# Kernel tuning notes

Hardware: AMD Instinct MI355X
Metric: run time of the kernel (lower is better)

Reference implementation:

```python
import jax, jax.numpy as jnp
import numpy as np
from jax import lax

N, M, T, IN, H, DEPTH = 64, 10, 160, 40, 256, 3
B = N * M
EPS = 1e-8


def setup_inputs() -> dict:
    key = jax.random.key(0)
    ks = jax.random.split(key, 20)
    s = 1.0 / np.sqrt(H)  # torch LSTM init scale
    inp = {
        "sequences": jax.random.normal(ks[0], (B, T, IN), jnp.float32),
        "len_sequences": jax.random.randint(ks[1], (B,), 80, T + 1, jnp.int32),
        "w_sim": jnp.float32(0.5),
        "b_sim": jnp.float32(0.5),
    }
    in_sizes = [IN, H, H]
    for l in range(DEPTH):
        k = 2 + 4 * l
        inp[f"Wih{l}"] = jax.random.uniform(ks[k], (4 * H, in_sizes[l]), jnp.float32, -s, s)
        inp[f"Whh{l}"] = jax.random.uniform(ks[k + 1], (4 * H, H), jnp.float32, -s, s)
        inp[f"bih{l}"] = jax.random.uniform(ks[k + 2], (4 * H,), jnp.float32, -s, s)
        inp[f"bhh{l}"] = jax.random.uniform(ks[k + 3], (4 * H,), jnp.float32, -s, s)
    return inp


def _lstm_layer(x_tbf, mask_tb, Wih, Whh, bih, bhh):
    """x_tbf: [T,B,F] time-major. mask_tb: [T,B] valid-step mask.
    Returns (h_seq [T,B,H], c_last [B,H]) where c_last is the cell state at
    the last valid timestep of each sequence (packed-sequence semantics)."""
    b = x_tbf.shape[1]
    h0 = jnp.zeros((b, H), x_tbf.dtype)
    c0 = jnp.zeros((b, H), x_tbf.dtype)

    def step(carry, xm):
        h, c = carry
        xt, mt = xm
        g = xt @ Wih.T + bih + h @ Whh.T + bhh  # [B,4H]
        i, f, gg, o = jnp.split(g, 4, axis=1)
        cn = jax.nn.sigmoid(f) * c + jax.nn.sigmoid(i) * jnp.tanh(gg)
        hn = jax.nn.sigmoid(o) * jnp.tanh(cn)
        m = mt[:, None]
        h2 = jnp.where(m, hn, h)
        c2 = jnp.where(m, cn, c)
        return (h2, c2), h2

    (hT, cT), h_seq = lax.scan(step, (h0, c0), (x_tbf, mask_tb))
    return h_seq, cT


def reference(sequences, len_sequences, Wih0, Whh0, bih0, bhh0,
              Wih1, Whh1, bih1, bhh1, Wih2, Whh2, bih2, bhh2,
              w_sim, b_sim):
    lens = len_sequences.astype(jnp.int32)
    x = jnp.transpose(sequences, (1, 0, 2))  # [T,B,IN]
    mask = jnp.arange(T)[:, None] < lens[None, :]  # [T,B]

    layers = [(Wih0, Whh0, bih0, bhh0), (Wih1, Whh1, bih1, bhh1), (Wih2, Whh2, bih2, bhh2)]
    c_last = None
    for (Wih, Whh, bih, bhh) in layers:
        x, c_last = _lstm_layer(x, mask, Wih, Whh, bih, bhh)
    E = c_last  # [B,H] final-layer cell state per utterance (original order)

    # L2-normalize embeddings (F.normalize, p=2, dim=1)
    E = E / jnp.maximum(jnp.linalg.norm(E, axis=1, keepdims=True), 1e-12)

    Er = E.reshape(N, M, H)
    C = Er.mean(axis=1)  # [N,H] speaker centroids
    # exclusive centroids exactly as source: (M*c_j + E_i)/(M-1)
    Cm = ((M * C[:, None, :] + Er) / (M - 1)).reshape(B, H)

    En = E / jnp.maximum(jnp.linalg.norm(E, axis=1, keepdims=True), EPS)
    Cn = C / jnp.maximum(jnp.linalg.norm(C, axis=1, keepdims=True), EPS)
    Cmn = Cm / jnp.maximum(jnp.linalg.norm(Cm, axis=1, keepdims=True), EPS)

    S = (En @ Cn.T) * w_sim + b_sim  # [B,N]: cos(E_i, c_j)*w + b

    # diagonal block: row i, col i//M uses exclusive centroid
    d = jnp.sum(En * Cmn, axis=1)  # [B]
    rows = jnp.arange(B)
    cols = jnp.repeat(jnp.arange(N), M)
    S = S.at[rows, cols].set(d * w_sim + b_sim)
    return S


if __name__ == "__main__":
    out = reference(**setup_inputs())
    print(out.shape, out.dtype)
```

## Files before the change

kernel.cpp:

```cpp
#include <hip/hip_runtime.h>
#include <cstdint>
#include <cstddef>

typedef __attribute__((ext_vector_type(8))) short short8;
typedef __attribute__((ext_vector_type(4))) float f32x4;
typedef __attribute__((ext_vector_type(4))) unsigned short us4;

#define N_SPK 64
#define M_UTT 10
#define T_SEQ 160
#define IN_F  40
#define H_DIM 256
#define B_TOT 640
#define G4    1024

__device__ __forceinline__ unsigned short f2bf(float f) {
  unsigned int u = __float_as_uint(f);
  u += 0x7FFFu + ((u >> 16) & 1u);
  return (unsigned short)(u >> 16);
}
__device__ __forceinline__ float b2f(unsigned short u) {
  return __uint_as_float(((unsigned int)u) << 16);
}
__device__ __forceinline__ float sigm(float x) {
  return 1.f / (1.f + __expf(-x));
}
__device__ __forceinline__ float tanh_fast(float x) {
  return 1.f - 2.f / (1.f + __expf(2.f * x));
}
__device__ __forceinline__ unsigned long long ato_ld(const unsigned long long* p) {
  return __hip_atomic_load(p, __ATOMIC_RELAXED, __HIP_MEMORY_SCOPE_AGENT);
}
__device__ __forceinline__ void ato_st(unsigned long long* p, unsigned long long v) {
  __hip_atomic_store(p, v, __ATOMIC_RELAXED, __HIP_MEMORY_SCOPE_AGENT);
}
__device__ __forceinline__ int flg_ld(const int* p) {
  return __hip_atomic_load(p, __ATOMIC_RELAXED, __HIP_MEMORY_SCOPE_AGENT);
}
__device__ __forceinline__ void flg_st(int* p, int v) {
  __hip_atomic_store(p, v, __ATOMIC_RELAXED, __HIP_MEMORY_SCOPE_AGENT);
}

__global__ void pack_w_kernel(const float* __restrict__ W, short* __restrict__ out,
                              int Kin, int Ktiles) {
  int idx = blockIdx.x * 256 + threadIdx.x;
  int total = 64 * Ktiles * 64;
  if (idx >= total) return;
  int lane = idx & 63;
  int rest = idx >> 6;
  int ks   = rest % Ktiles;
  int tile = rest / Ktiles;
  int n  = tile * 16 + (lane & 15);
  int k0 = ks * 32 + (lane >> 4) * 8;
  short8 v;
#pragma unroll
  for (int j = 0; j < 8; ++j) {
    int k = k0 + j;
    float f = (k < Kin) ? W[(size_t)n * Kin + k] : 0.f;
    v[j] = (short)f2bf(f);
  }
  *(short8*)&out[(size_t)idx * 8] = v;
}

__global__ void bias_sum_kernel(const float* __restrict__ a, const float* __restrict__ b,
                                float* __restrict__ o) {
  int i = blockIdx.x * 256 + threadIdx.x;
  if (i < G4) o[i] = a[i] + b[i];
}

__global__ __launch_bounds__(256, 2)
void gate_gemm0(const float* __restrict__ seq, const short* __restrict__ Wp,
                const float* __restrict__ bias, unsigned short* __restrict__ G) {
  const int btile = blockIdx.x % 40;
  const int rest  = blockIdx.x / 40;
  const int tg    = rest & 3;
  const int chunk = rest >> 2;
  const int tid = threadIdx.x, lane = tid & 63, wave = tid >> 6;
  const int nl = lane & 15, mq = lane >> 4;

  for (int mg = 0; mg < 4; ++mg) {
    const int t0 = chunk * 16 + mg * 4;
    f32x4 acc[4][4];
#pragma unroll
    for (int q = 0; q < 4; ++q) {
      int tile = tg * 16 + wave + 4 * q;
      float bv = bias[tile * 16 + nl];
#pragma unroll
      for (int mm = 0; mm < 4; ++mm) acc[mm][q] = (f32x4){bv, bv, bv, bv};
    }
    for (int kt = 0; kt < 2; ++kt) {
      short8 a[4];
      const int m = btile * 16 + nl;
      const int k0 = kt * 32 + mq * 8;
#pragma unroll
      for (int mm = 0; mm < 4; ++mm) {
#pragma unroll
        for (int j = 0; j < 8; ++j) {
          int k = k0 + j;
          float f = (k < IN_F) ? seq[((size_t)m * T_SEQ + (t0 + mm)) * IN_F + k] : 0.f;
          a[mm][j] = (short)f2bf(f);
        }
      }
#pragma unroll
      for (int q = 0; q < 4; ++q) {
        int tile = tg * 16 + wave + 4 * q;
        short8 b = *(const short8*)&Wp[(((size_t)tile * 2 + kt) * 64 + lane) * 8];
#pragma unroll
        for (int mm = 0; mm < 4; ++mm)
          acc[mm][q] = __builtin_amdgcn_mfma_f32_16x16x32_bf16(a[mm], b, acc[mm][q], 0, 0, 0);
      }
    }
#pragma unroll
    for (int mm = 0; mm < 4; ++mm)
#pragma unroll
      for (int q = 0; q < 4; ++q) {
        int tile = tg * 16 + wave + 4 * q;
        us4 o;
#pragma unroll
        for (int r = 0; r < 4; ++r) o[r] = f2bf(acc[mm][q][r]);
        *(us4*)&G[(((size_t)(t0 + mm) * 40 + btile) * 64 + tile) * 256 + lane * 4] = o;
      }
  }
}

template<int L>
__device__ __forceinline__ void rec_stage(
    int S, int hb,
    const short* __restrict__ Whhp, const short* __restrict__ Wihp,
    const unsigned short* __restrict__ G0, const float* __restrict__ biasl,
    unsigned long long* __restrict__ hxch, int* __restrict__ flags,
    const int* __restrict__ lens, float* __restrict__ c_state,
    unsigned short* h_sh, unsigned short* x_sh, float* c_sh,
    float* bias_sh, short* wih_lds, int* len_sh)
{
  const int tid = threadIdx.x, lane = tid & 63, wave = tid >> 6;
  const int mq = lane >> 4, nl = lane & 15;
  const int lc = wave * 16 + nl;
  const int colown = hb * 64 + lc;

  short8 wregH[4][8];
#pragma unroll
  for (int g = 0; g < 4; ++g) {
    const int tile = g * 16 + hb * 4 + wave;
#pragma unroll
    for (int kt = 0; kt < 8; ++kt)
      wregH[g][kt] = *(const short8*)&Whhp[(((size_t)tile * 8 + kt) * 64 + lane) * 8];
  }
  short8 wregI[4][4];
  if (L >= 1) {
#pragma unroll
    for (int g = 0; g < 4; ++g) {
      const int tile = g * 16 + hb * 4 + wave;
#pragma unroll
      for (int kt = 0; kt < 4; ++kt)
        wregI[g][kt] = *(const short8*)&Wihp[(((size_t)tile * 8 + kt) * 64 + lane) * 8];
    }
    for (int i = tid; i < 4096; i += 256) {
      int tl = i >> 6, ln = i & 63;
      int lt = tl >> 2, kt4 = tl & 3;
      int gt = (lt >> 2) * 16 + hb * 4 + (lt & 3);
      *(short8*)&wih_lds[(lt * 4 + kt4) * 512 + ln * 8] =
          *(const short8*)&Wihp[(((size_t)gt * 8 + 4 + kt4) * 64 + ln) * 8];
    }
    for (int i = tid; i < 1024; i += 256) bias_sh[i] = biasl[i];
  }
  for (int i = tid; i < 64 * 264; i += 256) h_sh[i] = 0;
  for (int i = tid; i < 64 * 65; i += 256) c_sh[i] = 0.f;
  if (tid < 64) len_sh[tid] = lens[S * 64 + tid];
  __syncthreads();

  const int fself = L * 40 + S * 4 + hb;

  for (int t = 0; t < T_SEQ; ++t) {
    const int par = t & 3;
    if (L >= 1 && tid < 4)
      while (flg_ld(&flags[(L - 1) * 40 + S * 4 + tid]) < t + 1) {}
    if (L < 2 && tid >= 4 && tid < 8)
      while (flg_ld(&flags[(L + 1) * 40 + S * 4 + (tid - 4)]) < t - 3) {}
    __syncthreads();

    unsigned long long xr[16];
    if (L >= 1) {
      const unsigned long long* xb =
          hxch + ((size_t)((par * 3 + (L - 1)) * 10 + S)) * 4096;
#pragma unroll
      for (int u = 0; u < 16; ++u) xr[u] = ato_ld(&xb[u * 256 + tid]);
    }
    f32x4 acc[4][4];
    if (L == 0) {
#pragma unroll
      for (int m = 0; m < 4; ++m)
#pragma unroll
        for (int g = 0; g < 4; ++g) {
          const int tile = g * 16 + hb * 4 + wave;
          us4 gv = *(const us4*)&G0[(((size_t)t * 40 + S * 4 + m) * 64 + tile) * 256 + lane * 4];
#pragma unroll
          for (int r = 0; r < 4; ++r) acc[m][g][r] = b2f(gv[r]);
        }
    } else {
#pragma unroll
      for (int g = 0; g < 4; ++g) {
        const int tile = g * 16 + hb * 4 + wave;
        float bv = bias_sh[tile * 16 + nl];
#pragma unroll
        for (int m = 0; m < 4; ++m) acc[m][g] = (f32x4){bv, bv, bv, bv};
      }
    }
#pragma unroll
    for (int kt = 0; kt < 8; ++kt) {
      short8 a[4];
#pragma unroll
      for (int m = 0; m < 4; ++m)
        a[m] = *(const short8*)&h_sh[(m * 16 + nl) * 264 + kt * 32 + mq * 8];
#pragma unroll
      for (int m = 0; m < 4; ++m)
#pragma unroll
        for (int g = 0; g < 4; ++g)
          acc[m][g] = __builtin_amdgcn_mfma_f32_16x16x32_bf16(a[m], wregH[g][kt], acc[m][g], 0, 0, 0);
    }
    if (L >= 1) {
#pragma unroll
      for (int u = 0; u < 16; ++u) {
        int j = u * 256 + tid, pp = j >> 10, jj = j & 1023;
        *(unsigned long long*)&x_sh[(jj >> 4) * 264 + pp * 64 + (jj & 15) * 4] = xr[u];
      }
      __syncthreads();
#pragma unroll
      for (int kt = 0; kt < 8; ++kt) {
        short8 a[4];
#pragma unroll
        for (int m = 0; m < 4; ++m)
          a[m] = *(const short8*)&x_sh[(m * 16 + nl) * 264 + kt * 32 + mq * 8];
#pragma unroll
        for (int g = 0; g < 4; ++g) {
          short8 b = (kt < 4) ? wregI[g][kt]
                              : *(const short8*)&wih_lds[((g * 4 + wave) * 4 + (kt - 4)) * 512 + lane * 8];
#pragma unroll
          for (int m = 0; m < 4; ++m)
            acc[m][g] = __builtin_amdgcn_mfma_f32_16x16x32_bf16(a[m], b, acc[m][g], 0, 0, 0);
        }
      }
    }
    unsigned short hv[16];
#pragma unroll
    for (int m = 0; m < 4; ++m)
#pragma unroll
      for (int r = 0; r < 4; ++r) {
        const int row = m * 16 + mq * 4 + r;
        float c_old = c_sh[row * 65 + lc];
        float cn = sigm(acc[m][1][r]) * c_old + sigm(acc[m][0][r]) * tanh_fast(acc[m][2][r]);
        float hn = sigm(acc[m][3][r]) * tanh_fast(cn);
        bool upd = t < len_sh[row];
        if (upd) c_sh[row * 65 + lc] = cn;
        hv[m * 4 + r] = upd ? f2bf(hn) : h_sh[row * 264 + colown];
      }
    __syncthreads();
#pragma unroll
    for (int m = 0; m < 4; ++m)
#pragma unroll
      for (int r = 0; r < 4; ++r)
        h_sh[(m * 16 + mq * 4 + r) * 264 + colown] = hv[m * 4 + r];
    __syncthreads();
    unsigned long long* myslab =
        hxch + ((size_t)((par * 3 + L) * 10 + S) * 4 + hb) * 1024;
    for (int j = tid; j < 1024; j += 256) {
      int sample = j >> 4, l4 = j & 15;
      unsigned long long v =
          *(const unsigned long long*)&h_sh[sample * 264 + hb * 64 + l4 * 4];
      ato_st(&myslab[j], v);
    }
    __syncthreads();
    if (tid == 0) flg_st(&flags[fself], t + 1);
    if (tid < 3) {
      int p = tid + (tid >= hb ? 1 : 0);
      while (flg_ld(&flags[L * 40 + S * 4 + p]) < t + 1) {}
    }
    __syncthreads();
    {
      unsigned long long pr[12];
#pragma unroll
      for (int u = 0; u < 12; ++u) {
        int j = u * 256 + tid;
        int pp = j >> 10, jj = j & 1023;
        int p = pp + (pp >= hb ? 1 : 0);
        pr[u] = ato_ld(&hxch[((size_t)((par * 3 + L) * 10 + S) * 4 + p) * 1024 + jj]);
      }
#pragma unroll
      for (int u = 0; u < 12; ++u) {
        int j = u * 256 + tid;
        int pp = j >> 10, jj = j & 1023;
        int p = pp + (pp >= hb ? 1 : 0);
        *(unsigned long long*)&h_sh[(jj >> 4) * 264 + p * 64 + (jj & 15) * 4] = pr[u];
      }
    }
    __syncthreads();
  }
  if (L == 2) {
#pragma unroll
    for (int m = 0; m < 4; ++m)
#pragma unroll
      for (int r = 0; r < 4; ++r) {
        const int row = m * 16 + mq * 4 + r;
        c_state[((size_t)S * 64 + row) * 256 + colown] = c_sh[row * 65 + lc];
      }
  }
}

__global__ __launch_bounds__(256, 1)
void fused_lstm(const short* __restrict__ Whhp_all, const short* __restrict__ Wih1p,
                const short* __restrict__ Wih2p, const float* __restrict__ biasc,
                const unsigned short* __restrict__ G0, const int* __restrict__ lens,
                unsigned long long* __restrict__ hxch, int* __restrict__ flags,
                float* __restrict__ c_state)
{
  __shared__ unsigned short h_sh[64 * 264];
  __shared__ unsigned short x_sh[64 * 264];
  __shared__ float c_sh[64 * 65];
  __shared__ float bias_sh[1024];
  __shared__ short wih_lds[16 * 4 * 512];
  __shared__ int len_sh[64];
  const int bid = blockIdx.x;
  const int L = bid / 40;
  const int S = (bid % 40) >> 2;
  const int hb = bid & 3;

  if (L == 0)
    rec_stage<0>(S, hb, Whhp_all,          nullptr, G0, nullptr,
                 hxch, flags, lens, c_state, h_sh, x_sh, c_sh, bias_sh, wih_lds, len_sh);
  else if (L == 1)
    rec_stage<1>(S, hb, Whhp_all + 262144, Wih1p, G0, biasc + G4,
                 hxch, flags, lens, c_state, h_sh, x_sh, c_sh, bias_sh, wih_lds, len_sh);
  else
    rec_stage<2>(S, hb, Whhp_all + 524288, Wih2p, G0, biasc + 2 * G4,
                 hxch, flags, lens, c_state, h_sh, x_sh, c_sh, bias_sh, wih_lds, len_sh);
}

__global__ void k_norm(const float* __restrict__ E, float* __restrict__ E1,
                       float* __restrict__ En) {
  int row  = blockIdx.x * 4 + (threadIdx.x >> 6);
  int lane = threadIdx.x & 63;
  const float* e = E + (size_t)row * H_DIM;
  float v[4]; float ss = 0.f;
#pragma unroll
  for (int j = 0; j < 4; ++j) { v[j] = e[lane + 64 * j]; ss += v[j] * v[j]; }
#pragma unroll
  for (int m = 32; m >= 1; m >>= 1) ss += __shfl_xor(ss, m, 64);
  float nrm  = sqrtf(ss);
  float inv1 = 1.f / fmaxf(nrm, 1e-12f);
  float inv2 = 1.f / fmaxf(nrm * inv1, 1e-8f);
#pragma unroll
  for (int j = 0; j < 4; ++j) {
    float e1 = v[j] * inv1;
    E1[(size_t)row * H_DIM + lane + 64 * j] = e1;
    En[(size_t)row * H_DIM + lane + 64 * j] = e1 * inv2;
  }
}

__global__ void k_cent(const float* __restrict__ E1, float* __restrict__ C,
                       float* __restrict__ CnT) {
  int n = blockIdx.x;
  int lane = threadIdx.x;
  float v[4]; float ss = 0.f;
#pragma unroll
  for (int j = 0; j < 4; ++j) {
    int col = lane + 64 * j;
    float s = 0.f;
    for (int m = 0; m < M_UTT; ++m) s += E1[((size_t)n * M_UTT + m) * H_DIM + col];
    v[j] = s / (float)M_UTT;
    ss += v[j] * v[j];
  }
#pragma unroll
  for (int m = 32; m >= 1; m >>= 1) ss += __shfl_xor(ss, m, 64);
  float inv = 1.f / fmaxf(sqrtf(ss), 1e-8f);
#pragma unroll
  for (int j = 0; j < 4; ++j) {
    int col = lane + 64 * j;
    C[(size_t)n * H_DIM + col]  = v[j];
    CnT[(size_t)col * N_SPK + n] = v[j] * inv;
  }
}

__global__ void k_cm(const float* __restrict__ E1, const float* __restrict__ C,
                     float* __restrict__ Cmn) {
  int b    = blockIdx.x * 4 + (threadIdx.x >> 6);
  int lane = threadIdx.x & 63;
  int spk  = b / M_UTT;
  float v[4]; float ss = 0.f;
#pragma unroll
  for (int j = 0; j < 4; ++j) {
    int col = lane + 64 * j;
    v[j] = ((float)M_UTT * C[(size_t)spk * H_DIM + col] + E1[(size_t)b * H_DIM + col])
           / (float)(M_UTT - 1);
    ss += v[j] * v[j];
  }
#pragma unroll
  for (int m = 32; m >= 1; m >>= 1) ss += __shfl_xor(ss, m, 64);
  float inv = 1.f / fmaxf(sqrtf(ss), 1e-8f);
#pragma unroll
  for (int j = 0; j < 4; ++j)
    Cmn[(size_t)b * H_DIM + lane + 64 * j] = v[j] * inv;
}

__global__ void k_sim(const float* __restrict__ En, const float* __restrict__ CnT,
                      const float* __restrict__ Cmn, const float* __restrict__ w_sim,
                      const float* __restrict__ b_sim, float* __restrict__ S) {
  int b = blockIdx.x;
  int n = threadIdx.x;
  int diag = b / M_UTT;
  float w = w_sim[0], bb = b_sim[0];
  float s = 0.f;
  for (int k = 0; k < H_DIM; ++k) {
    float en = En[(size_t)b * H_DIM + k];
    float c  = (n == diag) ? Cmn[(size_t)b * H_DIM + k] : CnT[(size_t)k * N_SPK + n];
    s += en * c;
  }
  S[(size_t)b * N_SPK + n] = s * w + bb;
}

#define O_WHH   0ull
#define O_WIH0  1572864ull
#define O_WIH1  1703936ull
#define O_WIH2  2228224ull
#define O_BIAS  2752512ull
#define O_CST   2764800ull
#define O_E1    3420160ull
#define O_EN    4075520ull
#define O_C     4730880ull
#define O_CNT   4796416ull
#define O_CMN   4861952ull
#define O_FLG   5517312ull
#define O_HXCH  5521408ull
#define O_G0    9453568ull

extern "C" void kernel_launch(void* const* d_in, const int* in_sizes, int n_in,
                              void* d_out, int out_size, void* d_ws, size_t ws_size,
                              hipStream_t stream) {
  const float* seq   = (const float*)d_in[0];
  const int*   lens  = (const int*)d_in[1];
  const float* w_sim = (const float*)d_in[2];
  const float* b_sim = (const float*)d_in[3];
  const float* Wih[3] = {(const float*)d_in[4],  (const float*)d_in[8],  (const float*)d_in[12]};
  const float* Whh[3] = {(const float*)d_in[5],  (const float*)d_in[9],  (const float*)d_in[13]};
  const float* bih[3] = {(const float*)d_in[6],  (const float*)d_in[10], (const float*)d_in[14]};
  const float* bhh[3] = {(const float*)d_in[7],  (const float*)d_in[11], (const float*)d_in[15]};

  char* ws = (char*)d_ws;
  short* Whhp_all = (short*)(ws + O_WHH);
  short* Wihp[3] = {(short*)(ws + O_WIH0), (short*)(ws + O_WIH1), (short*)(ws + O_WIH2)};
  float* biasc = (float*)(ws + O_BIAS);
  float* c_state = (float*)(ws + O_CST);
  float* E1  = (float*)(ws + O_E1);
  float* En  = (float*)(ws + O_EN);
  float* C   = (float*)(ws + O_C);
  float* CnT = (float*)(ws + O_CNT);
  float* Cmn = (float*)(ws + O_CMN);
  int* flags = (int*)(ws + O_FLG);
  unsigned long long* hxch = (unsigned long long*)(ws + O_HXCH);
  unsigned short* G0 = (unsigned short*)(ws + O_G0);
  float* S = (float*)d_out;

  pack_w_kernel<<<32, 256, 0, stream>>>(Wih[0], Wihp[0], IN_F, 2);
  pack_w_kernel<<<128, 256, 0, stream>>>(Whh[0], Whhp_all, H_DIM, 8);
  pack_w_kernel<<<128, 256, 0, stream>>>(Whh[1], Whhp_all + 262144, H_DIM, 8);
  pack_w_kernel<<<128, 256, 0, stream>>>(Whh[2], Whhp_all + 524288, H_DIM, 8);
  pack_w_kernel<<<128, 256, 0, stream>>>(Wih[1], Wihp[1], H_DIM, 8);
  pack_w_kernel<<<128, 256, 0, stream>>>(Wih[2], Wihp[2], H_DIM, 8);
  for (int l = 0; l < 3; ++l)
    bias_sum_kernel<<<4, 256, 0, stream>>>(bih[l], bhh[l], biasc + l * G4);

  gate_gemm0<<<1600, 256, 0, stream>>>(seq, Wihp[0], biasc, G0);

  hipMemsetAsync(ws + O_FLG, 0, 4096, stream);
  fused_lstm<<<120, 256, 0, stream>>>(Whhp_all, Wihp[1], Wihp[2], biasc, G0, lens,
                                      hxch, flags, c_state);

  k_norm<<<160, 256, 0, stream>>>(c_state, E1, En);
  k_cent<<<N_SPK, 64, 0, stream>>>(E1, C, CnT);
  k_cm<<<160, 256, 0, stream>>>(E1, C, Cmn);
  k_sim<<<B_TOT, 64, 0, stream>>>(En, CnT, Cmn, w_sim, b_sim, S);
}
```

Measured before the change: 1.740 ms.

## Publish h-slab from registers, pad flags, and add sleep in spin-waits

New measurement: 2.129 ms. 1.22x slower.

```diff
diff --git a/kernel.cpp b/kernel.cpp
--- a/kernel.cpp
+++ b/kernel.cpp
@@ -13,6 +13,7 @@
 #define H_DIM 256
 #define B_TOT 640
 #define G4    1024
+#define FSTR  64
 
 __device__ __forceinline__ unsigned short f2bf(float f) {
   unsigned int u = __float_as_uint(f);
@@ -174,9 +175,11 @@
   for (int t = 0; t < T_SEQ; ++t) {
     const int par = t & 3;
     if (L >= 1 && tid < 4)
-      while (flg_ld(&flags[(L - 1) * 40 + S * 4 + tid]) < t + 1) {}
+      while (flg_ld(&flags[((L - 1) * 40 + S * 4 + tid) * FSTR]) < t + 1)
+        __builtin_amdgcn_s_sleep(1);
     if (L < 2 && tid >= 4 && tid < 8)
-      while (flg_ld(&flags[(L + 1) * 40 + S * 4 + (tid - 4)]) < t - 3) {}
+      while (flg_ld(&flags[((L + 1) * 40 + S * 4 + (tid - 4)) * FSTR]) < t - 3)
+        __builtin_amdgcn_s_sleep(1);
     __syncthreads();
 
     unsigned long long xr[16];
@@ -222,7 +225,13 @@
 #pragma unroll
       for (int u = 0; u < 16; ++u) {
         int j = u * 256 + tid, pp = j >> 10, jj = j & 1023;
-        *(unsigned long long*)&x_sh[(jj >> 4) * 264 + pp * 64 + (jj & 15) * 4] = xr[u];
+        int col = pp * 64 + (jj >> 4);
+        int row0 = ((jj & 15) >> 2) * 16 + (jj & 3) * 4;
+        unsigned long long v = xr[u];
+        x_sh[(row0 + 0) * 264 + col] = (unsigned short)v;
+        x_sh[(row0 + 1) * 264 + col] = (unsigned short)(v >> 16);
+        x_sh[(row0 + 2) * 264 + col] = (unsigned short)(v >> 32);
+        x_sh[(row0 + 3) * 264 + col] = (unsigned short)(v >> 48);
       }
       __syncthreads();
 #pragma unroll
@@ -254,6 +263,19 @@
         if (upd) c_sh[row * 65 + lc] = cn;
         hv[m * 4 + r] = upd ? f2bf(hn) : h_sh[row * 264 + colown];
       }
+    {
+      unsigned long long* myslab =
+          hxch + ((size_t)((par * 3 + L) * 10 + S) * 4 + hb) * 1024;
+#pragma unroll
+      for (int m = 0; m < 4; ++m) {
+        unsigned long long v =
+            (unsigned long long)hv[m * 4 + 0] |
+            ((unsigned long long)hv[m * 4 + 1] << 16) |
+            ((unsigned long long)hv[m * 4 + 2] << 32) |
+            ((unsigned long long)hv[m * 4 + 3] << 48);
+        ato_st(&myslab[lc * 16 + m * 4 + mq], v);
+      }
+    }
     __syncthreads();
 #pragma unroll
     for (int m = 0; m < 4; ++m)
@@ -261,19 +283,11 @@
       for (int r = 0; r < 4; ++r)
         h_sh[(m * 16 + mq * 4 + r) * 264 + colown] = hv[m * 4 + r];
     __syncthreads();
-    unsigned long long* myslab =
-        hxch + ((size_t)((par * 3 + L) * 10 + S) * 4 + hb) * 1024;
-    for (int j = tid; j < 1024; j += 256) {
-      int sample = j >> 4, l4 = j & 15;
-      unsigned long long v =
-          *(const unsigned long long*)&h_sh[sample * 264 + hb * 64 + l4 * 4];
-      ato_st(&myslab[j], v);
-    }
-    __syncthreads();
-    if (tid == 0) flg_st(&flags[fself], t + 1);
+    if (tid == 0) flg_st(&flags[fself * FSTR], t + 1);
     if (tid < 3) {
       int p = tid + (tid >= hb ? 1 : 0);
-      while (flg_ld(&flags[L * 40 + S * 4 + p]) < t + 1) {}
+      while (flg_ld(&flags[(L * 40 + S * 4 + p) * FSTR]) < t + 1)
+        __builtin_amdgcn_s_sleep(1);
     }
     __syncthreads();
     {
@@ -290,7 +304,13 @@
         int j = u * 256 + tid;
         int pp = j >> 10, jj = j & 1023;
         int p = pp + (pp >= hb ? 1 : 0);
-        *(unsigned long long*)&h_sh[(jj >> 4) * 264 + p * 64 + (jj & 15) * 4] = pr[u];
+        int col = p * 64 + (jj >> 4);
+        int row0 = ((jj & 15) >> 2) * 16 + (jj & 3) * 4;
+        unsigned long long v = pr[u];
+        h_sh[(row0 + 0) * 264 + col] = (unsigned short)v;
+        h_sh[(row0 + 1) * 264 + col] = (unsigned short)(v >> 16);
+        h_sh[(row0 + 2) * 264 + col] = (unsigned short)(v >> 32);
+        h_sh[(row0 + 3) * 264 + col] = (unsigned short)(v >> 48);
       }
     }
     __syncthreads();
@@ -429,8 +449,8 @@
 #define O_CNT   4796416ull
 #define O_CMN   4861952ull
 #define O_FLG   5517312ull
-#define O_HXCH  5521408ull
-#define O_G0    9453568ull
+#define O_HXCH  5548032ull
+#define O_G0    9480192ull
 
 extern "C" void kernel_launch(void* const* d_in, const int* in_sizes, int n_in,
                               void* d_out, int out_size, void* d_ws, size_t ws_size,
@@ -470,7 +490,7 @@
 
   gate_gemm0<<<1600, 256, 0, stream>>>(seq, Wihp[0], biasc, G0);
 
-  hipMemsetAsync(ws + O_FLG, 0, 4096, stream);
+  hipMemsetAsync(ws + O_FLG, 0, 30720, stream);
   fused_lstm<<<120, 256, 0, stream>>>(Whhp_all, Wihp[1], Wihp[2], biasc, G0, lens,
                                       hxch, flags, c_state);
 
```

## Prefetch layer-0 gate inputs into LDS and pad sync flags to separate lines

Applied to the files above, without the earlier changes.

Measured after the change: 1.696 ms. 2.5% less time.

```diff
diff --git a/kernel.cpp b/kernel.cpp
--- a/kernel.cpp
+++ b/kernel.cpp
@@ -13,6 +13,7 @@
 #define H_DIM 256
 #define B_TOT 640
 #define G4    1024
+#define FSTR  64
 
 __device__ __forceinline__ unsigned short f2bf(float f) {
   unsigned int u = __float_as_uint(f);
@@ -137,6 +138,7 @@
   const int mq = lane >> 4, nl = lane & 15;
   const int lc = wave * 16 + nl;
   const int colown = hb * 64 + lc;
+  unsigned long long* x64 = (unsigned long long*)x_sh;
 
   short8 wregH[4][8];
 #pragma unroll
@@ -167,6 +169,20 @@
   for (int i = tid; i < 64 * 264; i += 256) h_sh[i] = 0;
   for (int i = tid; i < 64 * 65; i += 256) c_sh[i] = 0.f;
   if (tid < 64) len_sh[tid] = lens[S * 64 + tid];
+
+  if (L == 0) {
+    us4 tmp[16];
+#pragma unroll
+    for (int m = 0; m < 4; ++m)
+#pragma unroll
+      for (int g = 0; g < 4; ++g) {
+        const int tile = g * 16 + hb * 4 + wave;
+        tmp[m * 4 + g] = *(const us4*)&G0[(((size_t)0 * 40 + S * 4 + m) * 64 + tile) * 256 + lane * 4];
+      }
+#pragma unroll
+    for (int u = 0; u < 16; ++u)
+      x64[u * 256 + tid] = *(unsigned long long*)&tmp[u];
+  }
   __syncthreads();
 
   const int fself = L * 40 + S * 4 + hb;
@@ -174,9 +190,9 @@
   for (int t = 0; t < T_SEQ; ++t) {
     const int par = t & 3;
     if (L >= 1 && tid < 4)
-      while (flg_ld(&flags[(L - 1) * 40 + S * 4 + tid]) < t + 1) {}
+      while (flg_ld(&flags[((L - 1) * 40 + S * 4 + tid) * FSTR]) < t + 1) {}
     if (L < 2 && tid >= 4 && tid < 8)
-      while (flg_ld(&flags[(L + 1) * 40 + S * 4 + (tid - 4)]) < t - 3) {}
+      while (flg_ld(&flags[((L + 1) * 40 + S * 4 + (tid - 4)) * FSTR]) < t - 3) {}
     __syncthreads();
 
     unsigned long long xr[16];
@@ -192,8 +208,8 @@
       for (int m = 0; m < 4; ++m)
 #pragma unroll
         for (int g = 0; g < 4; ++g) {
-          const int tile = g * 16 + hb * 4 + wave;
-          us4 gv = *(const us4*)&G0[(((size_t)t * 40 + S * 4 + m) * 64 + tile) * 256 + lane * 4];
+          unsigned long long v = x64[(m * 4 + g) * 256 + tid];
+          us4 gv = *(us4*)&v;
 #pragma unroll
           for (int r = 0; r < 4; ++r) acc[m][g][r] = b2f(gv[r]);
         }
@@ -270,10 +286,24 @@
       ato_st(&myslab[j], v);
     }
     __syncthreads();
-    if (tid == 0) flg_st(&flags[fself], t + 1);
+    if (tid == 0) flg_st(&flags[fself * FSTR], t + 1);
+    if (L == 0) {
+      int tn = (t + 1 < T_SEQ) ? t + 1 : t;
+      us4 tmp[16];
+#pragma unroll
+      for (int m = 0; m < 4; ++m)
+#pragma unroll
+        for (int g = 0; g < 4; ++g) {
+          const int tile = g * 16 + hb * 4 + wave;
+          tmp[m * 4 + g] = *(const us4*)&G0[(((size_t)tn * 40 + S * 4 + m) * 64 + tile) * 256 + lane * 4];
+        }
+#pragma unroll
+      for (int u = 0; u < 16; ++u)
+        x64[u * 256 + tid] = *(unsigned long long*)&tmp[u];
+    }
     if (tid < 3) {
       int p = tid + (tid >= hb ? 1 : 0);
-      while (flg_ld(&flags[L * 40 + S * 4 + p]) < t + 1) {}
+      while (flg_ld(&flags[(L * 40 + S * 4 + p) * FSTR]) < t + 1) {}
     }
     __syncthreads();
     {
@@ -429,8 +459,8 @@
 #define O_CNT   4796416ull
 #define O_CMN   4861952ull
 #define O_FLG   5517312ull
-#define O_HXCH  5521408ull
-#define O_G0    9453568ull
+#define O_HXCH  5548032ull
+#define O_G0    9480192ull
 
 extern "C" void kernel_launch(void* const* d_in, const int* in_sizes, int n_in,
                               void* d_out, int out_size, void* d_ws, size_t ws_size,
@@ -470,7 +500,7 @@
 
   gate_gemm0<<<1600, 256, 0, stream>>>(seq, Wihp[0], biasc, G0);
 
-  hipMemsetAsync(ws + O_FLG, 0, 4096, stream);
+  hipMemsetAsync(ws + O_FLG, 0, 30720, stream);
   fused_lstm<<<120, 256, 0, stream>>>(Whhp_all, Wihp[1], Wihp[2], biasc, G0, lens,
                                       hxch, flags, c_state);
 
```
